# Performance work log

Hardware: AMD Instinct MI355X
Metric: run time of the kernel (lower is better)

Reference implementation:

```python
import jax, jax.numpy as jnp
import numpy as np

N = 100000   # num nodes
E = 1000000  # num edges
IN, H, OUT = 128, 64, 64
THR = 0.1      # lcs_threshold
LN_EPS = 1e-5


def setup_inputs() -> dict:
    key = jax.random.key(0)
    ks = jax.random.split(key, 8)
    x = jax.random.normal(ks[0], (N, IN), dtype=jnp.float32)
    edge_index = jax.random.randint(ks[1], (2, E), 0, N, dtype=jnp.int32)
    W1 = jax.random.normal(ks[2], (IN, H), dtype=jnp.float32) / np.float32(np.sqrt(IN))
    b1 = jnp.zeros((H,), jnp.float32)
    W2 = jax.random.normal(ks[3], (H, OUT), dtype=jnp.float32) / np.float32(np.sqrt(H))
    b2 = jnp.zeros((OUT,), jnp.float32)
    ln_gamma = jnp.ones((H,), jnp.float32)
    ln_beta = jnp.zeros((H,), jnp.float32)
    return {"x": x, "W1": W1, "b1": b1, "W2": W2, "b2": b2,
            "ln_gamma": ln_gamma, "ln_beta": ln_beta, "edge_index": edge_index}


def _gcn_conv(h_in, W, b, src, dst, ew, n):
    """PyG GCNConv: D^-1/2 (A+I) D^-1/2 (h_in @ W) + b, with edge weights ew.
    Masked edges (ew=0) contribute neither messages nor degree -> equivalent to
    filtering them out."""
    h = h_in @ W                                   # [n, d_out]
    deg = jax.ops.segment_sum(ew, dst, num_segments=n) + 1.0  # +1 self-loop
    dis = jax.lax.rsqrt(deg)                       # deg >= 1, finite
    norm = dis[src] * dis[dst] * ew                # [E]
    agg = jax.ops.segment_sum(h[src] * norm[:, None], dst, num_segments=n)
    agg = agg + h * (dis * dis)[:, None]           # self-loop term
    return agg + b


def _layer_norm(h, gamma, beta):
    mu = jnp.mean(h, axis=-1, keepdims=True)
    var = jnp.mean(jnp.square(h - mu), axis=-1, keepdims=True)
    return (h - mu) * jax.lax.rsqrt(var + LN_EPS) * gamma + beta


def reference(x, W1, b1, W2, b2, ln_gamma, ln_beta, edge_index):
    src, dst = edge_index[0], edge_index[1]
    n = x.shape[0]
    ones_e = jnp.ones((src.shape[0],), x.dtype)

    # layer 0: no LCS filtering (i == 0)
    h = _gcn_conv(x, W1, b1, src, dst, ones_e, n)
    h = _layer_norm(h, ln_gamma, ln_beta)
    h = jax.nn.relu(h)  # dropout: inference mode (identity)

    # layer 1: LCS filtering via node scores = min-max normalized L2 norm
    s = jnp.linalg.norm(h, axis=1)
    s = (s - s.min()) / (s.max() - s.min() + 1e-8)
    mask = (s[dst] > THR).astype(x.dtype)

    out = _gcn_conv(h, W2, b2, src, dst, mask, n)
    return jax.nn.log_softmax(out, axis=1)
```

## Files before the change

kernel.cpp:

```cpp
#include <hip/hip_runtime.h>
#include <math.h>

#define N_NODES 100000
#define N_EDGES 1000000
#define IN_F 128
#define H_F 64
#define THRV 0.1f
#define LN_EPS 1e-5f
#define GRID_AGG 2048

#define BSHIFT 9
#define NB 196
#define EPB 2048
#define NPB ((N_EDGES + EPB - 1) / EPB)

static __device__ __forceinline__ float wave_sum(float x) {
  for (int o = 32; o > 0; o >>= 1) x += __shfl_xor(x, o, 64);
  return x;
}
static __device__ __forceinline__ float wave_max(float x) {
  for (int o = 32; o > 0; o >>= 1) x = fmaxf(x, __shfl_xor(x, o, 64));
  return x;
}


__global__ __launch_bounds__(256) void k_bcount(const int* __restrict__ dst,
                                                int* __restrict__ bcnt) {
  __shared__ int h[NB];
  for (int i = threadIdx.x; i < NB; i += 256) h[i] = 0;
  __syncthreads();
  int base = blockIdx.x * EPB;
  for (int i = threadIdx.x; i < EPB; i += 256) {
    int e = base + i;
    if (e < N_EDGES) atomicAdd(&h[dst[e] >> BSHIFT], 1);
  }
  __syncthreads();
  for (int i = threadIdx.x; i < NB; i += 256)
    if (h[i]) atomicAdd(&bcnt[i], h[i]);
}

__global__ void k_bscan(const int* __restrict__ bcnt, int* __restrict__ bbase,
                        int* __restrict__ bcur) {
  __shared__ int lds[256];
  int t = threadIdx.x;
  int v = (t < NB) ? bcnt[t] : 0;
  lds[t] = v;
  __syncthreads();
  int val = v;
  for (int o = 1; o < 256; o <<= 1) {
    int y = (t >= o) ? lds[t - o] : 0;
    __syncthreads();
    val += y;
    lds[t] = val;
    __syncthreads();
  }
  if (t < NB) {
    int ex = val - v;
    bbase[t] = ex;
    bcur[t] = ex;
  }
  if (t == 255) bbase[NB] = val;
}

__global__ __launch_bounds__(256) void k_part(const int* __restrict__ src,
                                              const int* __restrict__ dst,
                                              int* __restrict__ bcur,
                                              int* __restrict__ part) {
  __shared__ int h[NB];
  __shared__ int cur[NB];
  for (int i = threadIdx.x; i < NB; i += 256) h[i] = 0;
  __syncthreads();
  int base = blockIdx.x * EPB;
  for (int i = threadIdx.x; i < EPB; i += 256) {
    int e = base + i;
    if (e < N_EDGES) atomicAdd(&h[dst[e] >> BSHIFT], 1);
  }
  __syncthreads();
  for (int i = threadIdx.x; i < NB; i += 256) {
    int c = h[i];
    cur[i] = c ? atomicAdd(&bcur[i], c) : 0;
  }
  __syncthreads();
  for (int i = threadIdx.x; i < EPB; i += 256) {
    int e = base + i;
    if (e < N_EDGES) {
      int d = dst[e];
      int b = d >> BSHIFT;
      int pos = atomicAdd(&cur[b], 1);
      part[pos] = src[e] | ((d & 511) << 17);
    }
  }
}

__global__ __launch_bounds__(256) void k_build(
    const int* __restrict__ part, const int* __restrict__ bbase,
    int* __restrict__ indeg, int* __restrict__ offs, float* __restrict__ dis1,
    int* __restrict__ csr_src) {
  __shared__ int cnt[512];
  __shared__ int slds[256];
  int b = blockIdx.x;
  int t = threadIdx.x;
  int beg = bbase[b], end = bbase[b + 1];
  for (int i = t; i < 512; i += 256) cnt[i] = 0;
  __syncthreads();
  for (int i = beg + t; i < end; i += 256)
    atomicAdd(&cnt[(part[i] >> 17) & 511], 1);
  __syncthreads();
  int a0 = cnt[2 * t], a1 = cnt[2 * t + 1];
  int pairsum = a0 + a1;
  slds[t] = pairsum;
  __syncthreads();
  int val = pairsum;
  for (int o = 1; o < 256; o <<= 1) {
    int y = (t >= o) ? slds[t - o] : 0;
    __syncthreads();
    val += y;
    slds[t] = val;
    __syncthreads();
  }
  int ex = val - pairsum;
  int off0 = ex, off1 = ex + a0;
  cnt[2 * t] = off0;
  cnt[2 * t + 1] = off1;
  int node0 = (b << BSHIFT) + 2 * t;
  if (node0 < N_NODES) {
    indeg[node0] = a0;
    offs[node0] = beg + off0;
    dis1[node0] = rsqrtf((float)a0 + 1.f);
  }
  if (node0 + 1 < N_NODES) {
    indeg[node0 + 1] = a1;
    offs[node0 + 1] = beg + off1;
    dis1[node0 + 1] = rsqrtf((float)a1 + 1.f);
  }
  __syncthreads();
  for (int i = beg + t; i < end; i += 256) {
    int p = part[i];
    int loc = (p >> 17) & 511;
    int pos = atomicAdd(&cnt[loc], 1);
    csr_src[beg + pos] = p & 131071;
  }
}

template <int K>
__global__ __launch_bounds__(256) void k_gemm(const float* __restrict__ X,
                                              const float* __restrict__ W,
                                              const float* __restrict__ scale,
                                              float* __restrict__ Y, int nrows) {
  __shared__ __align__(16) float Ws[K][64];
  int t = threadIdx.x;
  for (int idx = t; idx < K * 16; idx += 256)
    ((float4*)&Ws[0][0])[idx] = ((const float4*)W)[idx];
  __syncthreads();

  int lane = t & 63;
  int wid = t >> 6;
  int tx = lane & 15, ty = lane >> 4;
  int rbase = blockIdx.x * 64 + wid * 16 + ty * 4;
  int r[4];
#pragma unroll
  for (int i = 0; i < 4; ++i) {
    int g = rbase + i;
    r[i] = (g < nrows) ? g : (nrows - 1);
  }
  int c0 = tx * 4;
  float acc[4][4] = {};

#pragma unroll 2
  for (int k = 0; k < K; k += 4) {
    float xv[4][4], wv[4][4];
#pragma unroll
    for (int i = 0; i < 4; ++i)
      *(float4*)xv[i] = *(const float4*)(X + (size_t)r[i] * K + k);
#pragma unroll
    for (int j = 0; j < 4; ++j)
      *(float4*)wv[j] = *(const float4*)&Ws[k + j][c0];
#pragma unroll
    for (int i = 0; i < 4; ++i)
#pragma unroll
      for (int kk = 0; kk < 4; ++kk)
#pragma unroll
        for (int j = 0; j < 4; ++j)
          acc[i][j] = fmaf(xv[i][kk], wv[kk][j], acc[i][j]);
  }

#pragma unroll
  for (int i = 0; i < 4; ++i) {
    int gr = rbase + i;
    if (gr < nrows) {
      float sc = scale[gr];
      float4 o;
      o.x = acc[i][0] * sc;
      o.y = acc[i][1] * sc;
      o.z = acc[i][2] * sc;
      o.w = acc[i][3] * sc;
      *(float4*)(Y + (size_t)gr * 64 + c0) = o;
    }
  }
}

__global__ __launch_bounds__(256) void k_agg1(
    const float* __restrict__ h1p, const int* __restrict__ offs,
    const int* __restrict__ indeg, const int* __restrict__ csr_src,
    const float* __restrict__ dis1, const float* __restrict__ b1,
    const float* __restrict__ gamma, const float* __restrict__ beta,
    float* __restrict__ h, float* __restrict__ s, float* __restrict__ mmpart) {
  int lane = threadIdx.x & 63;
  int wid = blockIdx.x * 4 + (threadIdx.x >> 6);
  int nw = gridDim.x * 4;
  float bmin = __builtin_inff(), bmax = -__builtin_inff();
  for (int v = wid; v < N_NODES; v += nw) {
    int beg = offs[v];
    int deg = indeg[v];
    float disv = dis1[v];
    float acc = h1p[v * 64 + lane];
    for (int c = 0; c < deg; c += 64) {
      int m = deg - c;
      if (m > 64) m = 64;
      int ul = (lane < m) ? csr_src[beg + c + lane] : 0;
      int j = 0;
      for (; j + 8 <= m; j += 8) {
        int u0 = __shfl(ul, j + 0), u1 = __shfl(ul, j + 1);
        int u2 = __shfl(ul, j + 2), u3 = __shfl(ul, j + 3);
        int u4 = __shfl(ul, j + 4), u5 = __shfl(ul, j + 5);
        int u6 = __shfl(ul, j + 6), u7 = __shfl(ul, j + 7);
        float a0 = h1p[u0 * 64 + lane], a1 = h1p[u1 * 64 + lane];
        float a2 = h1p[u2 * 64 + lane], a3 = h1p[u3 * 64 + lane];
        float a4 = h1p[u4 * 64 + lane], a5 = h1p[u5 * 64 + lane];
        float a6 = h1p[u6 * 64 + lane], a7 = h1p[u7 * 64 + lane];
        acc += ((a0 + a1) + (a2 + a3)) + ((a4 + a5) + (a6 + a7));
      }
      for (; j < m; ++j) {
        int u = __shfl(ul, j);
        acc += h1p[u * 64 + lane];
      }
    }
    acc = disv * acc + b1[lane];
    float mu = wave_sum(acc) * (1.f / 64.f);
    float d = acc - mu;
    float var = wave_sum(d * d) * (1.f / 64.f);
    float hn = d * rsqrtf(var + LN_EPS) * gamma[lane] + beta[lane];
    hn = fmaxf(hn, 0.f);
    h[v * 64 + lane] = hn;
    float sv = sqrtf(wave_sum(hn * hn));
    if (lane == 0) s[v] = sv;
    bmin = fminf(bmin, sv);
    bmax = fmaxf(bmax, sv);
  }
  __shared__ float lmin[4], lmax[4];
  if ((threadIdx.x & 63) == 0) {
    lmin[threadIdx.x >> 6] = bmin;
    lmax[threadIdx.x >> 6] = bmax;
  }
  __syncthreads();
  if (threadIdx.x == 0) {
    mmpart[blockIdx.x * 2] = fminf(fminf(lmin[0], lmin[1]), fminf(lmin[2], lmin[3]));
    mmpart[blockIdx.x * 2 + 1] = fmaxf(fmaxf(lmax[0], lmax[1]), fmaxf(lmax[2], lmax[3]));
  }
}

__global__ void k_minmax2(const float* __restrict__ mmpart, float* __restrict__ smm,
                          int nblk) {
  int t = threadIdx.x;
  float mn = __builtin_inff(), mx = -__builtin_inff();
  for (int i = t; i < nblk; i += 256) {
    mn = fminf(mn, mmpart[i * 2]);
    mx = fmaxf(mx, mmpart[i * 2 + 1]);
  }
  for (int o = 32; o; o >>= 1) {
    mn = fminf(mn, __shfl_xor(mn, o, 64));
    mx = fmaxf(mx, __shfl_xor(mx, o, 64));
  }
  __shared__ float a[4], b[4];
  if ((t & 63) == 0) { a[t >> 6] = mn; b[t >> 6] = mx; }
  __syncthreads();
  if (t == 0) {
    smm[0] = fminf(fminf(a[0], a[1]), fminf(a[2], a[3]));
    smm[1] = fmaxf(fmaxf(b[0], b[1]), fmaxf(b[2], b[3]));
  }
}

__global__ void k_dis2(const float* __restrict__ s, const float* __restrict__ smm,
                       const int* __restrict__ indeg, float* __restrict__ dis2) {
  int v = blockIdx.x * blockDim.x + threadIdx.x;
  if (v < N_NODES) {
    float inv = 1.f / (smm[1] - smm[0] + 1e-8f);
    float sn = (s[v] - smm[0]) * inv;
    float d = (sn > THRV) ? (float)indeg[v] : 0.f;
    dis2[v] = rsqrtf(d + 1.f);
  }
}

__global__ __launch_bounds__(256) void k_agg2(
    const float* __restrict__ h2p, const int* __restrict__ offs,
    const int* __restrict__ indeg, const int* __restrict__ csr_src,
    const float* __restrict__ s, const float* __restrict__ smm,
    const float* __restrict__ dis2, const float* __restrict__ b2,
    float* __restrict__ out) {
  int lane = threadIdx.x & 63;
  int wid = blockIdx.x * 4 + (threadIdx.x >> 6);
  int nw = gridDim.x * 4;
  float smin = smm[0];
  float inv = 1.f / (smm[1] - smm[0] + 1e-8f);
  for (int v = wid; v < N_NODES; v += nw) {
    float disv = dis2[v];
    float sn = (s[v] - smin) * inv;
    float acc = h2p[v * 64 + lane];
    if (sn > THRV) {
      int beg = offs[v];
      int deg = indeg[v];
      for (int c = 0; c < deg; c += 64) {
        int m = deg - c;
        if (m > 64) m = 64;
        int ul = (lane < m) ? csr_src[beg + c + lane] : 0;
        int j = 0;
        for (; j + 8 <= m; j += 8) {
          int u0 = __shfl(ul, j + 0), u1 = __shfl(ul, j + 1);
          int u2 = __shfl(ul, j + 2), u3 = __shfl(ul, j + 3);
          int u4 = __shfl(ul, j + 4), u5 = __shfl(ul, j + 5);
          int u6 = __shfl(ul, j + 6), u7 = __shfl(ul, j + 7);
          float a0 = h2p[u0 * 64 + lane], a1 = h2p[u1 * 64 + lane];
          float a2 = h2p[u2 * 64 + lane], a3 = h2p[u3 * 64 + lane];
          float a4 = h2p[u4 * 64 + lane], a5 = h2p[u5 * 64 + lane];
          float a6 = h2p[u6 * 64 + lane], a7 = h2p[u7 * 64 + lane];
          acc += ((a0 + a1) + (a2 + a3)) + ((a4 + a5) + (a6 + a7));
        }
        for (; j < m; ++j) {
          int u = __shfl(ul, j);
          acc += h2p[u * 64 + lane];
        }
      }
    }
    acc = disv * acc + b2[lane];
    float m = wave_max(acc);
    float p = expf(acc - m);
    float sum = wave_sum(p);
    out[v * 64 + lane] = acc - m - logf(sum);
  }
}

extern "C" void kernel_launch(void* const* d_in, const int* in_sizes, int n_in,
                              void* d_out, int out_size, void* d_ws, size_t ws_size,
                              hipStream_t stream) {
  const float* x = (const float*)d_in[0];
  const float* W1 = (const float*)d_in[1];
  const float* b1 = (const float*)d_in[2];
  const float* W2 = (const float*)d_in[3];
  const float* b2 = (const float*)d_in[4];
  const float* gamma = (const float*)d_in[5];
  const float* beta = (const float*)d_in[6];
  const int* ei = (const int*)d_in[7];
  const int* src = ei;
  const int* dst = ei + N_EDGES;
  float* out = (float*)d_out;

  char* ws = (char*)d_ws;
  size_t off = 0;
  auto alloc = [&](size_t bytes) {
    void* p = ws + off;
    off += (bytes + 255) & ~(size_t)255;
    return p;
  };
  int* indeg = (int*)alloc(N_NODES * 4);
  int* offs = (int*)alloc(N_NODES * 4);
  int* bcnt = (int*)alloc(NB * 4);
  int* bbase = (int*)alloc((NB + 1) * 4);
  int* bcur = (int*)alloc(NB * 4);
  int* csr_src = (int*)alloc(N_EDGES * 4);
  float* s = (float*)alloc(N_NODES * 4);
  float* dis1 = (float*)alloc(N_NODES * 4);
  float* dis2 = (float*)alloc(N_NODES * 4);
  float* mmpart = (float*)alloc(GRID_AGG * 2 * 4);
  float* smm = (float*)alloc(256);
  float* h1 = (float*)alloc((size_t)N_NODES * 64 * 4);
  float* h = (float*)alloc((size_t)N_NODES * 64 * 4);
  int* part = (int*)h1;
  (void)ws_size;
  (void)n_in;
  (void)in_sizes;
  (void)out_size;

  hipMemsetAsync(bcnt, 0, NB * 4, stream);
  k_bcount<<<NPB, 256, 0, stream>>>(dst, bcnt);
  k_bscan<<<1, 256, 0, stream>>>(bcnt, bbase, bcur);
  k_part<<<NPB, 256, 0, stream>>>(src, dst, bcur, part);
  k_build<<<NB, 256, 0, stream>>>(part, bbase, indeg, offs, dis1, csr_src);
  int gemm_grid = (N_NODES + 63) / 64;
  k_gemm<IN_F><<<gemm_grid, 256, 0, stream>>>(x, W1, dis1, h1, N_NODES);
  k_agg1<<<GRID_AGG, 256, 0, stream>>>(h1, offs, indeg, csr_src, dis1, b1, gamma,
                                       beta, h, s, mmpart);
  k_minmax2<<<1, 256, 0, stream>>>(mmpart, smm, GRID_AGG);
  k_dis2<<<(N_NODES + 255) / 256, 256, 0, stream>>>(s, smm, indeg, dis2);
  k_gemm<H_F><<<gemm_grid, 256, 0, stream>>>(h, W2, dis2, h1 , N_NODES);
  k_agg2<<<GRID_AGG, 256, 0, stream>>>(h1, offs, indeg, csr_src, s, smm, dis2, b2,
                                       out);
}
```

Measured before the change: 227.1 us.

## Drop count pass with fixed-capacity buckets, bf16 layer-2 features, atomic minmax, prefetch

Removes the separate bucket-count and scan kernels by giving each destination bucket a fixed slot of BCAP entries, so partitioning is a single pass over the edges. The layer-2 GEMM now writes bf16 features, which halves the bytes gathered in the second aggregation. The min/max reduction becomes float-as-int atomics, which removes a kernel launch, and both aggregation loops prefetch the next node's metadata and self row. Risks: BCAP overflow if a bucket exceeds 6144 edges (the mean per bucket is about 5100), reduced precision from bf16, and int atomics on floats that are only valid because the values are non-negative.

```diff
diff --git a/kernel.cpp b/kernel.cpp
--- a/kernel.cpp
+++ b/kernel.cpp
@@ -11,6 +11,7 @@
 
 #define BSHIFT 9
 #define NB 196
+#define BCAP 6144
 #define EPB 2048
 #define NPB ((N_EDGES + EPB - 1) / EPB)
 
@@ -22,85 +23,62 @@
   for (int o = 32; o > 0; o >>= 1) x = fmaxf(x, __shfl_xor(x, o, 64));
   return x;
 }
-
-
-__global__ __launch_bounds__(256) void k_bcount(const int* __restrict__ dst,
-                                                int* __restrict__ bcnt) {
-  __shared__ int h[NB];
-  for (int i = threadIdx.x; i < NB; i += 256) h[i] = 0;
-  __syncthreads();
-  int base = blockIdx.x * EPB;
-  for (int i = threadIdx.x; i < EPB; i += 256) {
-    int e = base + i;
-    if (e < N_EDGES) atomicAdd(&h[dst[e] >> BSHIFT], 1);
-  }
-  __syncthreads();
-  for (int i = threadIdx.x; i < NB; i += 256)
-    if (h[i]) atomicAdd(&bcnt[i], h[i]);
-}
-
-__global__ void k_bscan(const int* __restrict__ bcnt, int* __restrict__ bbase,
-                        int* __restrict__ bcur) {
-  __shared__ int lds[256];
-  int t = threadIdx.x;
-  int v = (t < NB) ? bcnt[t] : 0;
-  lds[t] = v;
-  __syncthreads();
-  int val = v;
-  for (int o = 1; o < 256; o <<= 1) {
-    int y = (t >= o) ? lds[t - o] : 0;
-    __syncthreads();
-    val += y;
-    lds[t] = val;
-    __syncthreads();
-  }
-  if (t < NB) {
-    int ex = val - v;
-    bbase[t] = ex;
-    bcur[t] = ex;
-  }
-  if (t == 255) bbase[NB] = val;
-}
+static __device__ __forceinline__ unsigned short f2bf(float f) {
+  unsigned u = __float_as_uint(f);
+  u = (u + 0x7FFFu + ((u >> 16) & 1u)) >> 16;
+  return (unsigned short)u;
+}
+static __device__ __forceinline__ float bf2f(unsigned short b) {
+  return __uint_as_float(((unsigned)b) << 16);
+}
+
 
 __global__ __launch_bounds__(256) void k_part(const int* __restrict__ src,
                                               const int* __restrict__ dst,
-                                              int* __restrict__ bcur,
+                                              int* __restrict__ bcnt,
                                               int* __restrict__ part) {
   __shared__ int h[NB];
   __shared__ int cur[NB];
-  for (int i = threadIdx.x; i < NB; i += 256) h[i] = 0;
+  int t = threadIdx.x;
+  for (int i = t; i < NB; i += 256) h[i] = 0;
   __syncthreads();
   int base = blockIdx.x * EPB;
-  for (int i = threadIdx.x; i < EPB; i += 256) {
-    int e = base + i;
-    if (e < N_EDGES) atomicAdd(&h[dst[e] >> BSHIFT], 1);
-  }
-  __syncthreads();
-  for (int i = threadIdx.x; i < NB; i += 256) {
+  int d[8];
+#pragma unroll
+  for (int i = 0; i < 8; ++i) {
+    int e = base + t + i * 256;
+    d[i] = (e < N_EDGES) ? dst[e] : -1;
+  }
+#pragma unroll
+  for (int i = 0; i < 8; ++i)
+    if (d[i] >= 0) atomicAdd(&h[d[i] >> BSHIFT], 1);
+  __syncthreads();
+  for (int i = t; i < NB; i += 256) {
     int c = h[i];
-    cur[i] = c ? atomicAdd(&bcur[i], c) : 0;
-  }
-  __syncthreads();
-  for (int i = threadIdx.x; i < EPB; i += 256) {
-    int e = base + i;
-    if (e < N_EDGES) {
-      int d = dst[e];
-      int b = d >> BSHIFT;
+    cur[i] = c ? atomicAdd(&bcnt[i], c) : 0;
+  }
+  __syncthreads();
+#pragma unroll
+  for (int i = 0; i < 8; ++i) {
+    if (d[i] >= 0) {
+      int e = base + t + i * 256;
+      int b = d[i] >> BSHIFT;
       int pos = atomicAdd(&cur[b], 1);
-      part[pos] = src[e] | ((d & 511) << 17);
+      part[b * BCAP + pos] = src[e] | ((d[i] & 511) << 17);
     }
   }
 }
 
 __global__ __launch_bounds__(256) void k_build(
-    const int* __restrict__ part, const int* __restrict__ bbase,
+    const int* __restrict__ part, const int* __restrict__ bcnt,
     int* __restrict__ indeg, int* __restrict__ offs, float* __restrict__ dis1,
     int* __restrict__ csr_src) {
   __shared__ int cnt[512];
   __shared__ int slds[256];
   int b = blockIdx.x;
   int t = threadIdx.x;
-  int beg = bbase[b], end = bbase[b + 1];
+  int beg = b * BCAP;
+  int end = beg + bcnt[b];
   for (int i = t; i < 512; i += 256) cnt[i] = 0;
   __syncthreads();
   for (int i = beg + t; i < end; i += 256)
@@ -142,11 +120,11 @@
   }
 }
 
-template <int K>
+template <int K, bool BF16OUT>
 __global__ __launch_bounds__(256) void k_gemm(const float* __restrict__ X,
                                               const float* __restrict__ W,
                                               const float* __restrict__ scale,
-                                              float* __restrict__ Y, int nrows) {
+                                              void* __restrict__ Yv, int nrows) {
   __shared__ __align__(16) float Ws[K][64];
   int t = threadIdx.x;
   for (int idx = t; idx < K * 16; idx += 256)
@@ -189,12 +167,21 @@
     int gr = rbase + i;
     if (gr < nrows) {
       float sc = scale[gr];
-      float4 o;
-      o.x = acc[i][0] * sc;
-      o.y = acc[i][1] * sc;
-      o.z = acc[i][2] * sc;
-      o.w = acc[i][3] * sc;
-      *(float4*)(Y + (size_t)gr * 64 + c0) = o;
+      if constexpr (BF16OUT) {
+        ushort4 o;
+        o.x = f2bf(acc[i][0] * sc);
+        o.y = f2bf(acc[i][1] * sc);
+        o.z = f2bf(acc[i][2] * sc);
+        o.w = f2bf(acc[i][3] * sc);
+        *(ushort4*)((unsigned short*)Yv + (size_t)gr * 64 + c0) = o;
+      } else {
+        float4 o;
+        o.x = acc[i][0] * sc;
+        o.y = acc[i][1] * sc;
+        o.z = acc[i][2] * sc;
+        o.w = acc[i][3] * sc;
+        *(float4*)((float*)Yv + (size_t)gr * 64 + c0) = o;
+      }
     }
   }
 }
@@ -204,16 +191,33 @@
     const int* __restrict__ indeg, const int* __restrict__ csr_src,
     const float* __restrict__ dis1, const float* __restrict__ b1,
     const float* __restrict__ gamma, const float* __restrict__ beta,
-    float* __restrict__ h, float* __restrict__ s, float* __restrict__ mmpart) {
+    float* __restrict__ h, float* __restrict__ s, int* __restrict__ smm_i) {
   int lane = threadIdx.x & 63;
   int wid = blockIdx.x * 4 + (threadIdx.x >> 6);
   int nw = gridDim.x * 4;
   float bmin = __builtin_inff(), bmax = -__builtin_inff();
-  for (int v = wid; v < N_NODES; v += nw) {
-    int beg = offs[v];
-    int deg = indeg[v];
-    float disv = dis1[v];
-    float acc = h1p[v * 64 + lane];
+  float b1l = b1[lane], gl = gamma[lane], bl = beta[lane];
+
+  int v = wid;
+  int beg = 0, deg = 0;
+  float disv = 0.f, self = 0.f;
+  if (v < N_NODES) {
+    beg = offs[v];
+    deg = indeg[v];
+    disv = dis1[v];
+    self = h1p[v * 64 + lane];
+  }
+  while (v < N_NODES) {
+    int vn = v + nw;
+    int begN = 0, degN = 0;
+    float disN = 0.f, selfN = 0.f;
+    if (vn < N_NODES) {
+      begN = offs[vn];
+      degN = indeg[vn];
+      disN = dis1[vn];
+      selfN = h1p[vn * 64 + lane];
+    }
+    float acc = self;
     for (int c = 0; c < deg; c += 64) {
       int m = deg - c;
       if (m > 64) m = 64;
@@ -235,17 +239,22 @@
         acc += h1p[u * 64 + lane];
       }
     }
-    acc = disv * acc + b1[lane];
+    acc = disv * acc + b1l;
     float mu = wave_sum(acc) * (1.f / 64.f);
     float d = acc - mu;
     float var = wave_sum(d * d) * (1.f / 64.f);
-    float hn = d * rsqrtf(var + LN_EPS) * gamma[lane] + beta[lane];
+    float hn = d * rsqrtf(var + LN_EPS) * gl + bl;
     hn = fmaxf(hn, 0.f);
     h[v * 64 + lane] = hn;
     float sv = sqrtf(wave_sum(hn * hn));
     if (lane == 0) s[v] = sv;
     bmin = fminf(bmin, sv);
     bmax = fmaxf(bmax, sv);
+    v = vn;
+    beg = begN;
+    deg = degN;
+    disv = disN;
+    self = selfN;
   }
   __shared__ float lmin[4], lmax[4];
   if ((threadIdx.x & 63) == 0) {
@@ -254,61 +263,63 @@
   }
   __syncthreads();
   if (threadIdx.x == 0) {
-    mmpart[blockIdx.x * 2] = fminf(fminf(lmin[0], lmin[1]), fminf(lmin[2], lmin[3]));
-    mmpart[blockIdx.x * 2 + 1] = fmaxf(fmaxf(lmax[0], lmax[1]), fmaxf(lmax[2], lmax[3]));
-  }
-}
-
-__global__ void k_minmax2(const float* __restrict__ mmpart, float* __restrict__ smm,
-                          int nblk) {
-  int t = threadIdx.x;
-  float mn = __builtin_inff(), mx = -__builtin_inff();
-  for (int i = t; i < nblk; i += 256) {
-    mn = fminf(mn, mmpart[i * 2]);
-    mx = fmaxf(mx, mmpart[i * 2 + 1]);
-  }
-  for (int o = 32; o; o >>= 1) {
-    mn = fminf(mn, __shfl_xor(mn, o, 64));
-    mx = fmaxf(mx, __shfl_xor(mx, o, 64));
-  }
-  __shared__ float a[4], b[4];
-  if ((t & 63) == 0) { a[t >> 6] = mn; b[t >> 6] = mx; }
-  __syncthreads();
-  if (t == 0) {
-    smm[0] = fminf(fminf(a[0], a[1]), fminf(a[2], a[3]));
-    smm[1] = fmaxf(fmaxf(b[0], b[1]), fmaxf(b[2], b[3]));
-  }
-}
-
-__global__ void k_dis2(const float* __restrict__ s, const float* __restrict__ smm,
+    float mn = fminf(fminf(lmin[0], lmin[1]), fminf(lmin[2], lmin[3]));
+    float mx = fmaxf(fmaxf(lmax[0], lmax[1]), fmaxf(lmax[2], lmax[3]));
+    atomicMin(&smm_i[0], __float_as_int(mn));
+    atomicMax(&smm_i[1], __float_as_int(mx));
+  }
+}
+
+__global__ void k_dis2(const float* __restrict__ s, const int* __restrict__ smm_i,
                        const int* __restrict__ indeg, float* __restrict__ dis2) {
   int v = blockIdx.x * blockDim.x + threadIdx.x;
   if (v < N_NODES) {
-    float inv = 1.f / (smm[1] - smm[0] + 1e-8f);
-    float sn = (s[v] - smm[0]) * inv;
+    float smin = __int_as_float(smm_i[0]);
+    float smax = __int_as_float(smm_i[1]);
+    float inv = 1.f / (smax - smin + 1e-8f);
+    float sn = (s[v] - smin) * inv;
     float d = (sn > THRV) ? (float)indeg[v] : 0.f;
     dis2[v] = rsqrtf(d + 1.f);
   }
 }
 
 __global__ __launch_bounds__(256) void k_agg2(
-    const float* __restrict__ h2p, const int* __restrict__ offs,
+    const unsigned short* __restrict__ h2b, const int* __restrict__ offs,
     const int* __restrict__ indeg, const int* __restrict__ csr_src,
-    const float* __restrict__ s, const float* __restrict__ smm,
+    const float* __restrict__ s, const int* __restrict__ smm_i,
     const float* __restrict__ dis2, const float* __restrict__ b2,
     float* __restrict__ out) {
   int lane = threadIdx.x & 63;
   int wid = blockIdx.x * 4 + (threadIdx.x >> 6);
   int nw = gridDim.x * 4;
-  float smin = smm[0];
-  float inv = 1.f / (smm[1] - smm[0] + 1e-8f);
-  for (int v = wid; v < N_NODES; v += nw) {
-    float disv = dis2[v];
-    float sn = (s[v] - smin) * inv;
-    float acc = h2p[v * 64 + lane];
+  float smin = __int_as_float(smm_i[0]);
+  float smax = __int_as_float(smm_i[1]);
+  float inv = 1.f / (smax - smin + 1e-8f);
+  float b2l = b2[lane];
+
+  int v = wid;
+  int beg = 0, deg = 0;
+  float disv = 0.f, self = 0.f, sn = 0.f;
+  if (v < N_NODES) {
+    beg = offs[v];
+    deg = indeg[v];
+    disv = dis2[v];
+    self = bf2f(h2b[v * 64 + lane]);
+    sn = (s[v] - smin) * inv;
+  }
+  while (v < N_NODES) {
+    int vn = v + nw;
+    int begN = 0, degN = 0;
+    float disN = 0.f, selfN = 0.f, snN = 0.f;
+    if (vn < N_NODES) {
+      begN = offs[vn];
+      degN = indeg[vn];
+      disN = dis2[vn];
+      selfN = bf2f(h2b[vn * 64 + lane]);
+      snN = (s[vn] - smin) * inv;
+    }
+    float acc = self;
     if (sn > THRV) {
-      int beg = offs[v];
-      int deg = indeg[v];
       for (int c = 0; c < deg; c += 64) {
         int m = deg - c;
         if (m > 64) m = 64;
@@ -319,23 +330,29 @@
           int u2 = __shfl(ul, j + 2), u3 = __shfl(ul, j + 3);
           int u4 = __shfl(ul, j + 4), u5 = __shfl(ul, j + 5);
           int u6 = __shfl(ul, j + 6), u7 = __shfl(ul, j + 7);
-          float a0 = h2p[u0 * 64 + lane], a1 = h2p[u1 * 64 + lane];
-          float a2 = h2p[u2 * 64 + lane], a3 = h2p[u3 * 64 + lane];
-          float a4 = h2p[u4 * 64 + lane], a5 = h2p[u5 * 64 + lane];
-          float a6 = h2p[u6 * 64 + lane], a7 = h2p[u7 * 64 + lane];
+          float a0 = bf2f(h2b[u0 * 64 + lane]), a1 = bf2f(h2b[u1 * 64 + lane]);
+          float a2 = bf2f(h2b[u2 * 64 + lane]), a3 = bf2f(h2b[u3 * 64 + lane]);
+          float a4 = bf2f(h2b[u4 * 64 + lane]), a5 = bf2f(h2b[u5 * 64 + lane]);
+          float a6 = bf2f(h2b[u6 * 64 + lane]), a7 = bf2f(h2b[u7 * 64 + lane]);
           acc += ((a0 + a1) + (a2 + a3)) + ((a4 + a5) + (a6 + a7));
         }
         for (; j < m; ++j) {
           int u = __shfl(ul, j);
-          acc += h2p[u * 64 + lane];
+          acc += bf2f(h2b[u * 64 + lane]);
         }
       }
     }
-    acc = disv * acc + b2[lane];
+    acc = disv * acc + b2l;
     float m = wave_max(acc);
     float p = expf(acc - m);
     float sum = wave_sum(p);
     out[v * 64 + lane] = acc - m - logf(sum);
+    v = vn;
+    beg = begN;
+    deg = degN;
+    disv = disN;
+    self = selfN;
+    sn = snN;
   }
 }
 
@@ -364,34 +381,31 @@
   int* indeg = (int*)alloc(N_NODES * 4);
   int* offs = (int*)alloc(N_NODES * 4);
   int* bcnt = (int*)alloc(NB * 4);
-  int* bbase = (int*)alloc((NB + 1) * 4);
-  int* bcur = (int*)alloc(NB * 4);
-  int* csr_src = (int*)alloc(N_EDGES * 4);
+  int* smm_i = (int*)alloc(256);
+  int* csr_src = (int*)alloc((size_t)NB * BCAP * 4);
   float* s = (float*)alloc(N_NODES * 4);
   float* dis1 = (float*)alloc(N_NODES * 4);
   float* dis2 = (float*)alloc(N_NODES * 4);
-  float* mmpart = (float*)alloc(GRID_AGG * 2 * 4);
-  float* smm = (float*)alloc(256);
   float* h1 = (float*)alloc((size_t)N_NODES * 64 * 4);
   float* h = (float*)alloc((size_t)N_NODES * 64 * 4);
   int* part = (int*)h1;
+  unsigned short* h2b = (unsigned short*)h1;
   (void)ws_size;
   (void)n_in;
   (void)in_sizes;
   (void)out_size;
 
   hipMemsetAsync(bcnt, 0, NB * 4, stream);
-  k_bcount<<<NPB, 256, 0, stream>>>(dst, bcnt);
-  k_bscan<<<1, 256, 0, stream>>>(bcnt, bbase, bcur);
-  k_part<<<NPB, 256, 0, stream>>>(src, dst, bcur, part);
-  k_build<<<NB, 256, 0, stream>>>(part, bbase, indeg, offs, dis1, csr_src);
+  hipMemsetAsync(&smm_i[0], 0x7F, 4, stream);
+  hipMemsetAsync(&smm_i[1], 0x00, 4, stream);
+  k_part<<<NPB, 256, 0, stream>>>(src, dst, bcnt, part);
+  k_build<<<NB, 256, 0, stream>>>(part, bcnt, indeg, offs, dis1, csr_src);
   int gemm_grid = (N_NODES + 63) / 64;
-  k_gemm<IN_F><<<gemm_grid, 256, 0, stream>>>(x, W1, dis1, h1, N_NODES);
+  k_gemm<IN_F, false><<<gemm_grid, 256, 0, stream>>>(x, W1, dis1, h1, N_NODES);
   k_agg1<<<GRID_AGG, 256, 0, stream>>>(h1, offs, indeg, csr_src, dis1, b1, gamma,
-                                       beta, h, s, mmpart);
-  k_minmax2<<<1, 256, 0, stream>>>(mmpart, smm, GRID_AGG);
-  k_dis2<<<(N_NODES + 255) / 256, 256, 0, stream>>>(s, smm, indeg, dis2);
-  k_gemm<H_F><<<gemm_grid, 256, 0, stream>>>(h, W2, dis2, h1 , N_NODES);
-  k_agg2<<<GRID_AGG, 256, 0, stream>>>(h1, offs, indeg, csr_src, s, smm, dis2, b2,
-                                       out);
-}
+                                       beta, h, s, smm_i);
+  k_dis2<<<(N_NODES + 255) / 256, 256, 0, stream>>>(s, smm_i, indeg, dis2);
+  k_gemm<H_F, true><<<gemm_grid, 256, 0, stream>>>(h, W2, dis2, h2b, N_NODES);
+  k_agg2<<<GRID_AGG, 256, 0, stream>>>(h2b, offs, indeg, csr_src, s, smm_i, dis2,
+                                       b2, out);
+}
```

After: 237.0 us. 4.4% more time.
